# Kernel optimization log

Measured on AMD Instinct MI355X. Metric: run time of the kernel, lower is better.

The kernel has to match this reference:

```python
import jax, jax.numpy as jnp
import numpy as np
import math

EPS = 1e-8
H, DM, S = 16, 1024, 128  # heads, d_model, seq_len (== channels)
DK = DM // H


def _fq_act_uint8(x):
    # Brevitas Uint8ActPerTensorFloat: per-tensor unsigned 8-bit fake-quant (negatives clip to 0)
    s = jnp.maximum(jnp.max(x), EPS) / 255.0
    return jnp.clip(jnp.round(x / s), 0.0, 255.0) * s


def _fq_w_int8(w):
    # Int8 weight per-tensor, narrow range [-127, 127]
    s = jnp.maximum(jnp.max(jnp.abs(w)), EPS) / 127.0
    return jnp.clip(jnp.round(w / s), -127.0, 127.0) * s, s


def _fq_pc_int8(x, axis):
    # QuantIdentity: signed 8-bit fake-quant, per-channel scale along `axis` (abs-max stats)
    red = tuple(i for i in range(x.ndim) if i != axis)
    s = jnp.maximum(jnp.max(jnp.abs(x), axis=red, keepdims=True), EPS) / 127.0
    return jnp.clip(jnp.round(x / s), -128.0, 127.0) * s


def _quant_linear(x, W, b):
    # QuantLinear: uint8 input quant, int8 weight quant, Int32 bias quant (scale = s_in * s_w)
    s_in = jnp.maximum(jnp.max(x), EPS) / 255.0
    xq = jnp.clip(jnp.round(x / s_in), 0.0, 255.0) * s_in
    Wq, s_w = _fq_w_int8(W)
    s_b = s_in * s_w
    bq = jnp.round(b / s_b) * s_b
    return jnp.einsum('bsd,od->bso', xq, Wq) + bq


def setup_inputs() -> dict:
    key = jax.random.key(0)
    ks = jax.random.split(key, 12)
    B = 64
    std = 1.0 / math.sqrt(DM)
    inp = {
        'query': jax.random.normal(ks[0], (B, S, DM), jnp.float32),
        'key':   jax.random.normal(ks[1], (B, S, DM), jnp.float32),
        'value': jax.random.normal(ks[2], (B, S, DM), jnp.float32),
        'mask':  jnp.ones((B, S, S), jnp.int32),
    }
    for i, nm in enumerate(['q', 'k', 'v', 'o']):
        inp[f'W{nm}'] = jax.random.normal(ks[3 + i], (DM, DM), jnp.float32) * std
        inp[f'b{nm}'] = jax.random.normal(ks[7 + i], (DM,), jnp.float32) * 0.01
    return inp


def reference(query, key, value, mask, Wq, bq, Wk, bk, Wv, bv, Wo, bo):
    B = query.shape[0]
    # QuantLinear projections -> [B, h, S, d_k]
    def proj(x, W, b):
        return _quant_linear(x, W, b).reshape(B, S, H, DK).transpose(0, 2, 1, 3)
    q = proj(query, Wq, bq)
    k = proj(key, Wk, bk)
    v = proj(value, Wv, bv)

    # quantizer_1: per-channel on q rows (axis 2); quantizer_2: on k^T columns (axis 3)
    kt = jnp.swapaxes(k, -2, -1)  # [B, h, d_k, S]
    scores = jnp.matmul(_fq_pc_int8(q, 2), _fq_pc_int8(kt, 3)) / math.sqrt(DK)
    scores = jnp.where(mask[:, None, :, :] == 0, -1e9, scores)
    p_attn = jax.nn.softmax(scores, axis=-1)

    # quantizer_3: per-channel on p_attn columns (axis 3); quantizer_4: on v rows (axis 2)
    x = jnp.matmul(_fq_pc_int8(p_attn, 3), _fq_pc_int8(v, 2))  # [B, h, S, d_k]
    x = x.transpose(0, 2, 1, 3).reshape(B, S, DM)
    return _quant_linear(x, Wo, bo)
```

## Files before the change

kernel.cpp:

```cpp
#include <hip/hip_runtime.h>
#include <hip/hip_bf16.h>
#include <math.h>

typedef unsigned short u16;
typedef unsigned int u32;
typedef unsigned long long u64;
typedef signed char i8;

constexpr int NB = 64, NS = 128, NDM = 1024, NH = 16, NDK = 64;
constexpr int NM = NB * NS;
constexpr float QEPS = 1e-8f;

typedef __attribute__((ext_vector_type(8))) short short8;
typedef __attribute__((ext_vector_type(4))) float f32x4;
typedef __attribute__((ext_vector_type(4))) int i32x4;

__device__ __forceinline__ u32 fenc(float f) {
  u32 u = __float_as_uint(f);
  return (u & 0x80000000u) ? ~u : (u | 0x80000000u);
}
__device__ __forceinline__ float fdec(u32 u) {
  u = (u & 0x80000000u) ? (u & 0x7FFFFFFFu) : ~u;
  return __uint_as_float(u);
}
__device__ __forceinline__ u16 f2bf(float f) { return (u16)(__float_as_uint(f) >> 16); }
__device__ __forceinline__ float bf2f(u16 u) { return __uint_as_float(((u32)u) << 16); }

__device__ __forceinline__ void glds16(const void* g, void* l) {
  __builtin_amdgcn_global_load_lds(
      (const __attribute__((address_space(1))) void*)(unsigned long long)(uintptr_t)g,
      (__attribute__((address_space(3))) void*)(u32)(uintptr_t)l, 16, 0, 0);
}


__global__ void maskbits_kernel(const int* __restrict__ mask, u64* __restrict__ mb,
                                u32* __restrict__ scl) {
  if (blockIdx.x == 0) {
    for (int i = threadIdx.x; i < 2048; i += blockDim.x) scl[i] = 0u;
  }
  int row = blockIdx.x * 4 + (threadIdx.x >> 6);
  int lane = threadIdx.x & 63;
  const int* mrow = mask + (size_t)row * NS;
  u64 b0 = __ballot(mrow[lane] != 0);
  u64 b1 = __ballot(mrow[64 + lane] != 0);
  if (lane == 0) { mb[row * 2] = b0; mb[row * 2 + 1] = b1; }
}

__global__ void fused_max_kernel(const float* __restrict__ q, const float* __restrict__ k,
                                 const float* __restrict__ v, const float* __restrict__ w0,
                                 const float* __restrict__ w1, const float* __restrict__ w2,
                                 const float* __restrict__ w3, u32* __restrict__ sclu) {
  int y = blockIdx.y;
  const float* src; size_t n4; int ab;
  switch (y) {
    case 0: src = q; n4 = (size_t)NM * NDM / 4; ab = 0; break;
    case 1: src = k; n4 = (size_t)NM * NDM / 4; ab = 0; break;
    case 2: src = v; n4 = (size_t)NM * NDM / 4; ab = 0; break;
    case 3: src = w0; n4 = (size_t)NDM * NDM / 4; ab = 1; break;
    case 4: src = w1; n4 = (size_t)NDM * NDM / 4; ab = 1; break;
    case 5: src = w2; n4 = (size_t)NDM * NDM / 4; ab = 1; break;
    default: src = w3; n4 = (size_t)NDM * NDM / 4; ab = 1; break;
  }
  float m = -INFINITY;
  size_t stride = (size_t)gridDim.x * blockDim.x;
  for (size_t i = (size_t)blockIdx.x * blockDim.x + threadIdx.x; i < n4; i += stride) {
    float4 f = ((const float4*)src)[i];
    if (ab) { f.x = fabsf(f.x); f.y = fabsf(f.y); f.z = fabsf(f.z); f.w = fabsf(f.w); }
    m = fmaxf(m, fmaxf(fmaxf(f.x, f.y), fmaxf(f.z, f.w)));
  }
  for (int off = 32; off; off >>= 1) m = fmaxf(m, __shfl_down(m, off));
  __shared__ float sm[4];
  if ((threadIdx.x & 63) == 0) sm[threadIdx.x >> 6] = m;
  __syncthreads();
  if (threadIdx.x == 0) {
    float r = fmaxf(fmaxf(sm[0], sm[1]), fmaxf(sm[2], sm[3]));
    atomicMax(&sclu[y], fenc(r));
  }
}

__global__ __launch_bounds__(256)
void quant_w_i8_kernel(const float* __restrict__ w0, const float* __restrict__ w1,
                       const float* __restrict__ w2, const float* __restrict__ w3,
                       i8* __restrict__ dst, int* __restrict__ colsum,
                       const u32* __restrict__ sclu) {
  int y = blockIdx.y, row = blockIdx.x, tid = threadIdx.x;
  const float* src = (y == 0 ? w0 : y == 1 ? w1 : y == 2 ? w2 : w3) + (size_t)row * NDM;
  float s = fmaxf(fdec(sclu[3 + y]), QEPS) / 127.0f;
  float4 f = ((const float4*)src)[tid];
  int a = (int)fminf(fmaxf(rintf(f.x / s), -127.f), 127.f);
  int b = (int)fminf(fmaxf(rintf(f.y / s), -127.f), 127.f);
  int c = (int)fminf(fmaxf(rintf(f.z / s), -127.f), 127.f);
  int d = (int)fminf(fmaxf(rintf(f.w / s), -127.f), 127.f);
  ((int*)(dst + (size_t)y * NDM * NDM + (size_t)row * NDM))[tid] =
      (a & 255) | ((b & 255) << 8) | ((c & 255) << 16) | ((d & 255) << 24);
  int ssum = a + b + c + d;
  for (int off = 32; off; off >>= 1) ssum += __shfl_down(ssum, off);
  __shared__ int sm[4];
  if ((tid & 63) == 0) sm[tid >> 6] = ssum;
  __syncthreads();
  if (tid == 0) colsum[y * NDM + row] = sm[0] + sm[1] + sm[2] + sm[3];
}

__global__ void quant_a_kernel(const float* __restrict__ s0, const float* __restrict__ s1,
                               const float* __restrict__ s2, i8* __restrict__ dst,
                               const u32* __restrict__ sclu, int slot_base) {
  int y = blockIdx.y;
  const float* src = y == 0 ? s0 : y == 1 ? s1 : s2;
  i8* d = dst + (size_t)y * NM * NDM;
  float s = fmaxf(fdec(sclu[slot_base + y]), QEPS) / 255.0f;
  size_t n4 = (size_t)NM * NDM / 4;
  size_t stride = (size_t)gridDim.x * blockDim.x;
  for (size_t i = (size_t)blockIdx.x * blockDim.x + threadIdx.x; i < n4; i += stride) {
    float4 f = ((const float4*)src)[i];
    int a = (int)fminf(fmaxf(rintf(f.x / s), 0.f), 255.f) - 128;
    int b = (int)fminf(fmaxf(rintf(f.y / s), 0.f), 255.f) - 128;
    int c = (int)fminf(fmaxf(rintf(f.z / s), 0.f), 255.f) - 128;
    int e = (int)fminf(fmaxf(rintf(f.w / s), 0.f), 255.f) - 128;
    ((int*)d)[i] = (a & 255) | ((b & 255) << 8) | ((c & 255) << 16) | ((e & 255) << 24);
  }
}

__global__ void qkv_i8_kernel(const float* __restrict__ projbase, i8* __restrict__ dstbase,
                              const float* __restrict__ scl) {
  int y = blockIdx.y;
  const float* src = projbase + (size_t)y * NM * NDM;
  i8* dst = dstbase + (size_t)y * NM * NDM;
  const float* sb = scl + 8 + y * 128;
  size_t n4 = (size_t)NM * NDM / 4;
  size_t stride = (size_t)gridDim.x * blockDim.x;
  for (size_t i = (size_t)blockIdx.x * blockDim.x + threadIdx.x; i < n4; i += stride) {
    int s_idx = (int)((i >> 8) & 127);
    float s = fmaxf(sb[s_idx], QEPS) / 127.0f;
    float4 f = ((const float4*)src)[i];
    int a = (int)fminf(fmaxf(rintf(f.x / s), -128.f), 127.f);
    int b = (int)fminf(fmaxf(rintf(f.y / s), -128.f), 127.f);
    int c = (int)fminf(fmaxf(rintf(f.z / s), -128.f), 127.f);
    int d = (int)fminf(fmaxf(rintf(f.w / s), -128.f), 127.f);
    ((int*)dst)[i] = (a & 255) | ((b & 255) << 8) | ((c & 255) << 16) | ((d & 255) << 24);
  }
}

constexpr int BM = 128, BN = 64, BK = 64, KTILES = NDM / BK;

template <bool PROJ>
__global__ __launch_bounds__(256, 4)
void gemm_kernel(const i8* __restrict__ Abase, const i8* __restrict__ Wbase,
                 const int* __restrict__ colsum, const float* __restrict__ b0,
                 const float* __restrict__ b1, const float* __restrict__ b2,
                 float* __restrict__ Cbase, u32* __restrict__ sclu,
                 float* __restrict__ rmax_part) {
  constexpr int K = NDM, N = NDM;
  const int z = PROJ ? blockIdx.z : 0;
  const i8* A = Abase + (size_t)z * NM * NDM;
  const i8* Wt = PROJ ? (Wbase + (size_t)z * NDM * NDM) : Wbase;
  const float* bias = PROJ ? (z == 0 ? b0 : z == 1 ? b1 : b2) : b0;
  float* C = PROJ ? (Cbase + (size_t)z * NM * NDM) : Cbase;
  const u32* slot_in = PROJ ? (sclu + z) : (sclu + 7);
  const u32* slot_w = PROJ ? (sclu + 3 + z) : (sclu + 6);
  const int* cs = colsum + (PROJ ? z : 3) * NDM;

  __shared__ __align__(16) i8 As[2][BM][BK];
  __shared__ __align__(16) i8 Bs[2][BN][BK];
  __shared__ float rmax2[4][64];

  const int tid = threadIdx.x;
  const int lane = tid & 63, wave = tid >> 6;
  const int wm = (wave & 1) * 64, wn = (wave >> 1) * 32;
  const int r16 = lane & 15, quad = lane >> 4;
  const int bm = blockIdx.x * BM, bn = blockIdx.y * BN;

  const int lrow = lane >> 2, lcol = (lane & 3) * 16;
  const i8* Ab = A + (size_t)(bm + wave * 32 + lrow) * K + lcol;
  const i8* Bb = Wt + (size_t)(bn + wave * 16 + lrow) * K + lcol;

  i32x4 acc[4][2] = {};

  glds16(Ab, &As[0][wave * 32][0]);
  glds16(Ab + (size_t)16 * K, &As[0][wave * 32 + 16][0]);
  glds16(Bb, &Bs[0][wave * 16][0]);
  __syncthreads();

  int cur = 0;
  for (int t = 0; t < KTILES; t++) {
    if (t + 1 < KTILES) {
      int k0 = (t + 1) * BK;
      glds16(Ab + k0, &As[cur ^ 1][wave * 32][0]);
      glds16(Ab + (size_t)16 * K + k0, &As[cur ^ 1][wave * 32 + 16][0]);
      glds16(Bb + k0, &Bs[cur ^ 1][wave * 16][0]);
    }
    i32x4 af[4], bfr[2];
#pragma unroll
    for (int i = 0; i < 4; i++)
      af[i] = *(const i32x4*)(&As[cur][wm + i * 16 + r16][quad * 16]);
#pragma unroll
    for (int j = 0; j < 2; j++)
      bfr[j] = *(const i32x4*)(&Bs[cur][wn + j * 16 + r16][quad * 16]);
#pragma unroll
    for (int i = 0; i < 4; i++)
#pragma unroll
      for (int j = 0; j < 2; j++)
        acc[i][j] = __builtin_amdgcn_mfma_i32_16x16x64_i8(af[i], bfr[j], acc[i][j], 0, 0, 0);
    __syncthreads();
    cur ^= 1;
  }

  float s_in = fmaxf(fdec(*slot_in), QEPS) / 255.0f;
  float s_w = fmaxf(fdec(*slot_w), QEPS) / 127.0f;
  float sc = s_in * s_w;

  float bq[2];
  int csj[2];
#pragma unroll
  for (int j = 0; j < 2; j++) {
    int gc = bn + wn + j * 16 + r16;
    bq[j] = rintf(bias[gc] / sc) * sc;
    csj[j] = cs[gc] << 7;
  }
#pragma unroll
  for (int i = 0; i < 4; i++) {
#pragma unroll
    for (int r = 0; r < 4; r++) {
      int l64 = i * 16 + quad * 4 + r;
      int gr = bm + wm + l64;
      float rm = 0.0f;
#pragma unroll
      for (int j = 0; j < 2; j++) {
        int gc = bn + wn + j * 16 + r16;
        float val = (float)(acc[i][j][r] + csj[j]) * sc + bq[j];
        C[(size_t)gr * N + gc] = val;
        if (PROJ) rm = fmaxf(rm, fabsf(val));
      }
      if (PROJ) {
#pragma unroll
        for (int off = 1; off < 16; off <<= 1) rm = fmaxf(rm, __shfl_xor(rm, off));
        if (r16 == 0) rmax2[wave][l64] = rm;
      }
    }
  }
  if (PROJ) {
    __syncthreads();
    if (tid < BM) {
      int g = tid >> 6, l = tid & 63;
      float m = fmaxf(rmax2[g][l], rmax2[g + 2][l]);
      int blockId = z * 1024 + blockIdx.x * 16 + blockIdx.y;
      rmax_part[(size_t)blockId * 128 + tid] = m;
    }
  }
}

__global__ void rmax_reduce_kernel(const float* __restrict__ part, u32* __restrict__ sclu) {
  int slot = blockIdx.x;
  int z = slot >> 7, lr = slot & 127;
  const float* base = part + (size_t)z * 1024 * 128 + lr;
  float m = 0.0f;
  for (int i = threadIdx.x; i < 1024; i += blockDim.x) m = fmaxf(m, base[(size_t)i * 128]);
  for (int off = 32; off; off >>= 1) m = fmaxf(m, __shfl_down(m, off));
  __shared__ float sm[4];
  if ((threadIdx.x & 63) == 0) sm[threadIdx.x >> 6] = m;
  __syncthreads();
  if (threadIdx.x == 0)
    sclu[8 + slot] = __float_as_uint(fmaxf(fmaxf(sm[0], sm[1]), fmaxf(sm[2], sm[3])));
}

__global__ __launch_bounds__(256)
void attn_colmax_kernel(const i8* __restrict__ qi8, const i8* __restrict__ ki8,
                        const u64* __restrict__ mb, const float* __restrict__ scl,
                        float* __restrict__ cm_part) {
  const int bh = blockIdx.x, b = bh >> 4, h = bh & 15;
  const int tid = threadIdx.x, lane = tid & 63, wave = tid >> 6;
  const int r16 = lane & 15, quad = lane >> 4;

  __shared__ __align__(16) i8 Qs[NS][80];
  __shared__ __align__(16) i8 Ks[NS][80];
  __shared__ float sqv[NS], skv[NS];
  __shared__ float cmw[4][NS];

  {
    int row = tid >> 1, half = (tid & 1) * 32;
    const i8* qp = qi8 + (size_t)(b * NS + row) * NDM + h * NDK + half;
    const i8* kp = ki8 + (size_t)(b * NS + row) * NDM + h * NDK + half;
    *(int4*)&Qs[row][half] = *(const int4*)qp;
    *(int4*)&Qs[row][half + 16] = *(const int4*)(qp + 16);
    *(int4*)&Ks[row][half] = *(const int4*)kp;
    *(int4*)&Ks[row][half + 16] = *(const int4*)(kp + 16);
    if (tid < NS) {
      sqv[tid] = fmaxf(scl[8 + tid], QEPS) / 127.0f;
      skv[tid] = fmaxf(scl[8 + 128 + tid], QEPS) / 127.0f;
    }
  }
  __syncthreads();

  const int rowbase = wave * 32;
  i32x4 acc[2][8] = {};
#pragma unroll
  for (int mt = 0; mt < 2; mt++) {
    i32x4 a = *(const i32x4*)&Qs[rowbase + mt * 16 + r16][quad * 16];
#pragma unroll
    for (int nt = 0; nt < 8; nt++) {
      i32x4 bfrag = *(const i32x4*)&Ks[nt * 16 + r16][quad * 16];
      acc[mt][nt] = __builtin_amdgcn_mfma_i32_16x16x64_i8(a, bfrag, acc[mt][nt], 0, 0, 0);
    }
  }

  float skc[8], cm[8];
#pragma unroll
  for (int nt = 0; nt < 8; nt++) { skc[nt] = skv[nt * 16 + r16]; cm[nt] = 0.0f; }

#pragma unroll
  for (int mt = 0; mt < 2; mt++) {
#pragma unroll
    for (int r = 0; r < 4; r++) {
      int row = rowbase + mt * 16 + quad * 4 + r;
      float sq = sqv[row];
      const u64* mrow = mb + ((size_t)b * NS + row) * 2;
      u64 m0 = mrow[0], m1 = mrow[1];
      float vals[8];
      float mx = -INFINITY;
#pragma unroll
      for (int nt = 0; nt < 8; nt++) {
        float v = (float)acc[mt][nt][r] * (sq * skc[nt]) * 0.125f;
        u64 bits = nt < 4 ? m0 : m1;
        if (((bits >> ((nt * 16 + r16) & 63)) & 1ull) == 0) v = -1e9f;
        vals[nt] = v;
        mx = fmaxf(mx, v);
      }
#pragma unroll
      for (int off = 1; off < 16; off <<= 1) mx = fmaxf(mx, __shfl_xor(mx, off));
      float sum = 0.0f;
#pragma unroll
      for (int nt = 0; nt < 8; nt++) { vals[nt] = __expf(vals[nt] - mx); sum += vals[nt]; }
#pragma unroll
      for (int off = 1; off < 16; off <<= 1) sum += __shfl_xor(sum, off);
#pragma unroll
      for (int nt = 0; nt < 8; nt++) {
        float p = vals[nt] / sum;
        cm[nt] = fmaxf(cm[nt], p);
      }
    }
  }

#pragma unroll
  for (int nt = 0; nt < 8; nt++) {
    float c = cm[nt];
    c = fmaxf(c, __shfl_xor(c, 16));
    c = fmaxf(c, __shfl_xor(c, 32));
    if (quad == 0) cmw[wave][nt * 16 + r16] = c;
  }
  __syncthreads();
  if (tid < NS) {
    float c = fmaxf(fmaxf(cmw[0][tid], cmw[1][tid]), fmaxf(cmw[2][tid], cmw[3][tid]));
    cm_part[(size_t)tid * (NB * NH) + bh] = c;
  }
}

__global__ void colmax_reduce_kernel(const float* __restrict__ cm_part,
                                     u32* __restrict__ sclu) {
  int j = blockIdx.x;
  const float* row = cm_part + (size_t)j * (NB * NH);
  float m = 0.0f;
  for (int i = threadIdx.x; i < NB * NH; i += blockDim.x) m = fmaxf(m, row[i]);
  for (int off = 32; off; off >>= 1) m = fmaxf(m, __shfl_down(m, off));
  __shared__ float sm[4];
  if ((threadIdx.x & 63) == 0) sm[threadIdx.x >> 6] = m;
  __syncthreads();
  if (threadIdx.x == 0)
    sclu[392 + j] = __float_as_uint(fmaxf(fmaxf(sm[0], sm[1]), fmaxf(sm[2], sm[3])));
}

__global__ __launch_bounds__(256, 4)
void attn_pv2_kernel(const i8* __restrict__ qi8, const i8* __restrict__ ki8,
                     const i8* __restrict__ vi8, const u64* __restrict__ mb,
                     const float* __restrict__ scl, float* __restrict__ xout,
                     u32* __restrict__ xmax_slot) {
  const int bh = blockIdx.x, b = bh >> 4, h = bh & 15;
  const int tid = threadIdx.x, lane = tid & 63, wave = tid >> 6;
  const int r16 = lane & 15, quad = lane >> 4;
  const int rowbase = wave * 32;

  union SU {
    i8 K[NS][64];
    struct { u16 hi[64][72]; u16 lo[64][72]; } v;
  };
  __shared__ __align__(16) SU u;
  __shared__ __align__(16) u16 Ps[NS][72];
  __shared__ float sqv[NS], skv[NS], spv[NS], svv[NS];
  __shared__ float xmw[4];

  const int jl = tid >> 2, d0v = (tid & 3) * 16;
  const i8* vb = vi8 + (size_t)(b * NS + jl) * NDM + h * NDK + d0v;
  int4 vpre0 = *(const int4*)vb;
  int4 vpre1 = *(const int4*)(vb + (size_t)64 * NDM);

  i32x4 aq[2];
  {
    const i8* qp = qi8 + (size_t)b * NS * NDM + h * NDK;
#pragma unroll
    for (int mt = 0; mt < 2; mt++)
      aq[mt] = *(const i32x4*)(qp + (size_t)(rowbase + mt * 16 + r16) * NDM + quad * 16);
    const int lrow = lane >> 2, lcol = (lane & 3) * 16;
#pragma unroll
    for (int p = 0; p < 2; p++) {
      int r = wave * 32 + p * 16;
      glds16(ki8 + (size_t)(b * NS + r + lrow) * NDM + h * NDK + lcol, &u.K[r][0]);
    }
    if (tid < NS) {
      sqv[tid] = fmaxf(scl[8 + tid], QEPS) / 127.0f;
      skv[tid] = fmaxf(scl[8 + 128 + tid], QEPS) / 127.0f;
      spv[tid] = fmaxf(scl[392 + tid], QEPS) / 127.0f;
      svv[tid] = fmaxf(scl[8 + 256 + tid], QEPS) / 127.0f;
    }
  }
  __syncthreads();

  i32x4 acc[2][8] = {};
  __builtin_amdgcn_s_setprio(1);
#pragma unroll
  for (int mt = 0; mt < 2; mt++) {
#pragma unroll
    for (int nt = 0; nt < 8; nt++) {
      i32x4 bfrag = *(const i32x4*)&u.K[nt * 16 + r16][quad * 16];
      acc[mt][nt] = __builtin_amdgcn_mfma_i32_16x16x64_i8(aq[mt], bfrag, acc[mt][nt], 0, 0, 0);
    }
  }
  __builtin_amdgcn_s_setprio(0);

  float skc[8], spc[8];
#pragma unroll
  for (int nt = 0; nt < 8; nt++) {
    skc[nt] = skv[nt * 16 + r16];
    spc[nt] = spv[nt * 16 + r16];
  }

  u32 pqh[2][4][2];
#pragma unroll
  for (int mt = 0; mt < 2; mt++) {
#pragma unroll
    for (int r = 0; r < 4; r++) {
      int row = rowbase + mt * 16 + quad * 4 + r;
      float sq = sqv[row];
      const u64* mrow = mb + ((size_t)b * NS + row) * 2;
      u64 m0 = mrow[0], m1 = mrow[1];
      float vals[8];
      float mx = -INFINITY;
#pragma unroll
      for (int nt = 0; nt < 8; nt++) {
        float v = (float)acc[mt][nt][r] * (sq * skc[nt]) * 0.125f;
        u64 bits = nt < 4 ? m0 : m1;
        if (((bits >> ((nt * 16 + r16) & 63)) & 1ull) == 0) v = -1e9f;
        vals[nt] = v;
        mx = fmaxf(mx, v);
      }
#pragma unroll
      for (int off = 1; off < 16; off <<= 1) mx = fmaxf(mx, __shfl_xor(mx, off));
      float sum = 0.0f;
#pragma unroll
      for (int nt = 0; nt < 8; nt++) { vals[nt] = __expf(vals[nt] - mx); sum += vals[nt]; }
#pragma unroll
      for (int off = 1; off < 16; off <<= 1) sum += __shfl_xor(sum, off);
#pragma unroll
      for (int nt = 0; nt < 4; nt++) {
        float p = vals[nt] / sum;
        float pq = fminf(fmaxf(rintf(p / spc[nt]), -128.f), 127.f);
        Ps[row][nt * 16 + r16] = f2bf(pq);
      }
#pragma unroll
      for (int n2 = 0; n2 < 2; n2++) {
        float pa_ = vals[4 + n2 * 2] / sum;
        float pb_ = vals[5 + n2 * 2] / sum;
        float qa = fminf(fmaxf(rintf(pa_ / spc[4 + n2 * 2]), -128.f), 127.f);
        float qb = fminf(fmaxf(rintf(pb_ / spc[5 + n2 * 2]), -128.f), 127.f);
        pqh[mt][r][n2] = (u32)f2bf(qa) | ((u32)f2bf(qb) << 16);
      }
    }
  }

  f32x4 xacc[2][4] = {};
#pragma unroll
  for (int half = 0; half < 2; half++) {
    __syncthreads();
    {
      int j = half * 64 + jl;
      float g = spv[j] * svv[j];
      int4 raw = half ? vpre1 : vpre0;
      const i8* rb = (const i8*)&raw;
#pragma unroll
      for (int d = 0; d < 16; d++) {
        float w = (float)rb[d] * g;
        u16 hi = f2bf(w);
        u.v.hi[d0v + d][jl] = hi;
        u.v.lo[d0v + d][jl] = f2bf(w - bf2f(hi));
      }
    }
    __syncthreads();
    __builtin_amdgcn_s_setprio(1);
#pragma unroll
    for (int kk = 0; kk < 2; kk++) {
      short8 pa[2];
#pragma unroll
      for (int mt = 0; mt < 2; mt++)
        pa[mt] = *(const short8*)&Ps[rowbase + mt * 16 + r16][kk * 32 + quad * 8];
#pragma unroll
      for (int nt = 0; nt < 4; nt++) {
        short8 vh = *(const short8*)&u.v.hi[nt * 16 + r16][kk * 32 + quad * 8];
        short8 vl = *(const short8*)&u.v.lo[nt * 16 + r16][kk * 32 + quad * 8];
#pragma unroll
        for (int mt = 0; mt < 2; mt++) {
          xacc[mt][nt] = __builtin_amdgcn_mfma_f32_16x16x32_bf16(pa[mt], vh, xacc[mt][nt], 0, 0, 0);
          xacc[mt][nt] = __builtin_amdgcn_mfma_f32_16x16x32_bf16(pa[mt], vl, xacc[mt][nt], 0, 0, 0);
        }
      }
    }
    __builtin_amdgcn_s_setprio(0);
    if (half == 0) {
#pragma unroll
      for (int mt = 0; mt < 2; mt++)
#pragma unroll
        for (int r = 0; r < 4; r++) {
          int row = rowbase + mt * 16 + quad * 4 + r;
#pragma unroll
          for (int n2 = 0; n2 < 2; n2++) {
            u32 pk = pqh[mt][r][n2];
            Ps[row][(n2 * 2) * 16 + r16] = (u16)(pk & 0xFFFFu);
            Ps[row][(n2 * 2 + 1) * 16 + r16] = (u16)(pk >> 16);
          }
        }
    }
  }

  float mx = -INFINITY;
#pragma unroll
  for (int mt = 0; mt < 2; mt++)
#pragma unroll
    for (int nt = 0; nt < 4; nt++)
#pragma unroll
      for (int r = 0; r < 4; r++) {
        int row = rowbase + mt * 16 + quad * 4 + r;
        xout[((size_t)b * NS + row) * NDM + h * NDK + nt * 16 + r16] = xacc[mt][nt][r];
        mx = fmaxf(mx, xacc[mt][nt][r]);
      }
#pragma unroll
  for (int off = 1; off < 64; off <<= 1) mx = fmaxf(mx, __shfl_xor(mx, off));
  if (lane == 0) xmw[wave] = mx;
  __syncthreads();
  if (tid == 0) {
    float m = fmaxf(fmaxf(xmw[0], xmw[1]), fmaxf(xmw[2], xmw[3]));
    atomicMax(xmax_slot, fenc(m));
  }
}

constexpr size_t OFF_SCL = 0;
constexpr size_t OFF_CS  = 8192;
constexpr size_t OFF_MB  = OFF_CS + 4 * NDM * 4;
constexpr size_t OFF_W   = OFF_MB + (size_t)NM * 16;
constexpr size_t OFF_XQ  = OFF_W + 4 * (size_t)NDM * NDM;
constexpr size_t OFF_PQ  = OFF_XQ + 3 * (size_t)NM * NDM;
constexpr size_t OFF_I8  = OFF_PQ + 3 * (size_t)NM * NDM * 4;
constexpr size_t OFF_CM  = OFF_I8 + 3 * (size_t)NM * NDM;
constexpr size_t OFF_RP  = OFF_CM + (size_t)NS * NB * NH * 4;

extern "C" void kernel_launch(void* const* d_in, const int* in_sizes, int n_in,
                              void* d_out, int out_size, void* d_ws, size_t ws_size,
                              hipStream_t stream) {
  const float* query = (const float*)d_in[0];
  const float* key = (const float*)d_in[1];
  const float* value = (const float*)d_in[2];
  const int* mask = (const int*)d_in[3];
  const float* Wq = (const float*)d_in[4]; const float* bq = (const float*)d_in[5];
  const float* Wk = (const float*)d_in[6]; const float* bk = (const float*)d_in[7];
  const float* Wv = (const float*)d_in[8]; const float* bv = (const float*)d_in[9];
  const float* Wo = (const float*)d_in[10]; const float* bo = (const float*)d_in[11];

  char* ws = (char*)d_ws;
  float* scl = (float*)(ws + OFF_SCL);
  u32* sclu = (u32*)scl;
  int* colsum = (int*)(ws + OFF_CS);
  u64* mb = (u64*)(ws + OFF_MB);
  i8* wb = (i8*)(ws + OFF_W);
  i8* wob = wb + 3 * (size_t)NDM * NDM;
  i8* xq = (i8*)(ws + OFF_XQ);
  float* proj = (float*)(ws + OFF_PQ);
  i8* qkv8 = (i8*)(ws + OFF_I8);
  float* cm_part = (float*)(ws + OFF_CM);
  float* rmax_part = (float*)(ws + OFF_RP);
  float* xout = proj + 2 * (size_t)NM * NDM;
  i8* vi8 = qkv8 + 2 * (size_t)NM * NDM;

  maskbits_kernel<<<NM / 4, 256, 0, stream>>>(mask, mb, sclu);
  fused_max_kernel<<<dim3(512, 7), 256, 0, stream>>>(query, key, value, Wq, Wk, Wv, Wo, sclu);
  quant_w_i8_kernel<<<dim3(NDM, 4), 256, 0, stream>>>(Wq, Wk, Wv, Wo, wb, colsum, sclu);
  quant_a_kernel<<<dim3(512, 3), 256, 0, stream>>>(query, key, value, xq, sclu, 0);

  gemm_kernel<true><<<dim3(NM / BM, NDM / BN, 3), 256, 0, stream>>>(
      xq, wb, colsum, bq, bk, bv, proj, sclu, rmax_part);
  rmax_reduce_kernel<<<384, 256, 0, stream>>>(rmax_part, sclu);

  qkv_i8_kernel<<<dim3(512, 3), 256, 0, stream>>>(proj, qkv8, scl);

  attn_colmax_kernel<<<NB * NH, 256, 0, stream>>>(qkv8, qkv8 + (size_t)NM * NDM, mb, scl,
                                                  cm_part);
  colmax_reduce_kernel<<<NS, 256, 0, stream>>>(cm_part, sclu);
  attn_pv2_kernel<<<NB * NH, 256, 0, stream>>>(qkv8, qkv8 + (size_t)NM * NDM, vi8, mb, scl,
                                               xout, sclu + 7);

  quant_a_kernel<<<dim3(512, 1), 256, 0, stream>>>(xout, xout, xout, xq, sclu, 7);
  gemm_kernel<false><<<dim3(NM / BM, NDM / BN, 1), 256, 0, stream>>>(
      xq, wob, colsum, bo, bo, bo, (float*)d_out, sclu, rmax_part);
}
```

Measured before the change: 390.9 us.

## Fuse attention colmax, reduce, and PV into one cooperative kernel

Replaces the three attention launches (QK colmax, column-max reduce, PV) with a single cooperative kernel that keeps QK^T probabilities in registers across two grid-wide syncs. This avoids recomputing QK^T and softmax in the PV pass and removes two kernel launches. The cost is grid synchronization overhead and a requirement that all 1024 blocks be co-resident (at least 4 per CU). If that fails, the old three-kernel path is used.

```diff
diff --git a/kernel.cpp b/kernel.cpp
--- a/kernel.cpp
+++ b/kernel.cpp
@@ -1,6 +1,9 @@
 #include <hip/hip_runtime.h>
 #include <hip/hip_bf16.h>
+#include <hip/hip_cooperative_groups.h>
 #include <math.h>
+
+namespace cg = cooperative_groups;
 
 typedef unsigned short u16;
 typedef unsigned int u32;
@@ -262,6 +265,243 @@
     sclu[8 + slot] = __float_as_uint(fmaxf(fmaxf(sm[0], sm[1]), fmaxf(sm[2], sm[3])));
 }
 
+__global__ __launch_bounds__(256, 4)
+void attn_fused_kernel(const i8* __restrict__ qi8, const i8* __restrict__ ki8,
+                       const i8* __restrict__ vi8, const u64* __restrict__ mb,
+                       const float* __restrict__ scl, u32* __restrict__ sclu,
+                       float* __restrict__ cm_part, float* __restrict__ xout,
+                       u32* __restrict__ xmax_slot) {
+  const int bh = blockIdx.x, b = bh >> 4, h = bh & 15;
+  const int tid = threadIdx.x, lane = tid & 63, wave = tid >> 6;
+  const int r16 = lane & 15, quad = lane >> 4;
+  const int rowbase = wave * 32;
+
+  union SU {
+    struct { i8 K[NS][64]; float cmw[4][NS]; } qk;
+    struct { u16 hi[64][72]; u16 lo[64][72]; } v;
+  };
+  __shared__ __align__(16) SU u;
+  __shared__ __align__(16) u16 Ps[NS][72];
+  __shared__ float sqv[NS], skv[NS], svv[NS], spv[NS];
+  __shared__ float xmw[4];
+
+  const int jl = tid >> 2, d0v = (tid & 3) * 16;
+  const i8* vb = vi8 + (size_t)(b * NS + jl) * NDM + h * NDK + d0v;
+  int4 vpre0 = *(const int4*)vb;
+  int4 vpre1 = *(const int4*)(vb + (size_t)64 * NDM);
+
+  i32x4 aq[2];
+  {
+    const i8* qp = qi8 + (size_t)b * NS * NDM + h * NDK;
+#pragma unroll
+    for (int mt = 0; mt < 2; mt++)
+      aq[mt] = *(const i32x4*)(qp + (size_t)(rowbase + mt * 16 + r16) * NDM + quad * 16);
+    const int lrow = lane >> 2, lcol = (lane & 3) * 16;
+#pragma unroll
+    for (int p = 0; p < 2; p++) {
+      int r = wave * 32 + p * 16;
+      glds16(ki8 + (size_t)(b * NS + r + lrow) * NDM + h * NDK + lcol, &u.qk.K[r][0]);
+    }
+    if (tid < NS) {
+      sqv[tid] = fmaxf(scl[8 + tid], QEPS) / 127.0f;
+      skv[tid] = fmaxf(scl[8 + 128 + tid], QEPS) / 127.0f;
+      svv[tid] = fmaxf(scl[8 + 256 + tid], QEPS) / 127.0f;
+    }
+  }
+  __syncthreads();
+
+  i32x4 acc[2][8] = {};
+  __builtin_amdgcn_s_setprio(1);
+#pragma unroll
+  for (int mt = 0; mt < 2; mt++) {
+#pragma unroll
+    for (int nt = 0; nt < 8; nt++) {
+      i32x4 bfrag = *(const i32x4*)&u.qk.K[nt * 16 + r16][quad * 16];
+      acc[mt][nt] = __builtin_amdgcn_mfma_i32_16x16x64_i8(aq[mt], bfrag, acc[mt][nt], 0, 0, 0);
+    }
+  }
+  __builtin_amdgcn_s_setprio(0);
+
+  float skc[8];
+#pragma unroll
+  for (int nt = 0; nt < 8; nt++) skc[nt] = skv[nt * 16 + r16];
+
+  float p[2][4][8];
+  float cm[8] = {0.f, 0.f, 0.f, 0.f, 0.f, 0.f, 0.f, 0.f};
+#pragma unroll
+  for (int mt = 0; mt < 2; mt++) {
+#pragma unroll
+    for (int r = 0; r < 4; r++) {
+      int row = rowbase + mt * 16 + quad * 4 + r;
+      float sq = sqv[row];
+      const u64* mrow = mb + ((size_t)b * NS + row) * 2;
+      u64 m0 = mrow[0], m1 = mrow[1];
+      float vals[8];
+      float mx = -INFINITY;
+#pragma unroll
+      for (int nt = 0; nt < 8; nt++) {
+        float v = (float)acc[mt][nt][r] * (sq * skc[nt]) * 0.125f;
+        u64 bits = nt < 4 ? m0 : m1;
+        if (((bits >> ((nt * 16 + r16) & 63)) & 1ull) == 0) v = -1e9f;
+        vals[nt] = v;
+        mx = fmaxf(mx, v);
+      }
+#pragma unroll
+      for (int off = 1; off < 16; off <<= 1) mx = fmaxf(mx, __shfl_xor(mx, off));
+      float sum = 0.0f;
+#pragma unroll
+      for (int nt = 0; nt < 8; nt++) { vals[nt] = __expf(vals[nt] - mx); sum += vals[nt]; }
+#pragma unroll
+      for (int off = 1; off < 16; off <<= 1) sum += __shfl_xor(sum, off);
+#pragma unroll
+      for (int nt = 0; nt < 8; nt++) {
+        float pv_ = vals[nt] / sum;
+        p[mt][r][nt] = pv_;
+        cm[nt] = fmaxf(cm[nt], pv_);
+      }
+    }
+  }
+
+#pragma unroll
+  for (int nt = 0; nt < 8; nt++) {
+    float c = cm[nt];
+    c = fmaxf(c, __shfl_xor(c, 16));
+    c = fmaxf(c, __shfl_xor(c, 32));
+    if (quad == 0) u.qk.cmw[wave][nt * 16 + r16] = c;
+  }
+  __syncthreads();
+  if (tid < NS) {
+    float c = fmaxf(fmaxf(u.qk.cmw[0][tid], u.qk.cmw[1][tid]),
+                    fmaxf(u.qk.cmw[2][tid], u.qk.cmw[3][tid]));
+    __hip_atomic_store(&cm_part[(size_t)bh * NS + tid], c, __ATOMIC_RELAXED,
+                       __HIP_MEMORY_SCOPE_AGENT);
+  }
+
+  cg::this_grid().sync();
+
+  if (bh < NS) {
+    float m = 0.0f;
+    for (int i = tid; i < NB * NH; i += 256)
+      m = fmaxf(m, __hip_atomic_load(&cm_part[(size_t)i * NS + bh], __ATOMIC_RELAXED,
+                                     __HIP_MEMORY_SCOPE_AGENT));
+#pragma unroll
+    for (int off = 32; off; off >>= 1) m = fmaxf(m, __shfl_down(m, off));
+    if (lane == 0) xmw[wave] = m;
+    __syncthreads();
+    if (tid == 0) {
+      float mm = fmaxf(fmaxf(xmw[0], xmw[1]), fmaxf(xmw[2], xmw[3]));
+      __hip_atomic_store(&sclu[1024 + bh], __float_as_uint(mm), __ATOMIC_RELAXED,
+                         __HIP_MEMORY_SCOPE_AGENT);
+    }
+  }
+
+  cg::this_grid().sync();
+
+  if (tid < NS) {
+    u32 cu = __hip_atomic_load(&sclu[1024 + tid], __ATOMIC_RELAXED,
+                               __HIP_MEMORY_SCOPE_AGENT);
+    spv[tid] = fmaxf(__uint_as_float(cu), QEPS) / 127.0f;
+  }
+  __syncthreads();
+
+  float spc[8];
+#pragma unroll
+  for (int nt = 0; nt < 8; nt++) spc[nt] = spv[nt * 16 + r16];
+
+  u32 pqh[2][4][2];
+#pragma unroll
+  for (int mt = 0; mt < 2; mt++) {
+#pragma unroll
+    for (int r = 0; r < 4; r++) {
+      int row = rowbase + mt * 16 + quad * 4 + r;
+#pragma unroll
+      for (int nt = 0; nt < 4; nt++) {
+        float pq = fminf(fmaxf(rintf(p[mt][r][nt] / spc[nt]), -128.f), 127.f);
+        Ps[row][nt * 16 + r16] = f2bf(pq);
+      }
+#pragma unroll
+      for (int n2 = 0; n2 < 2; n2++) {
+        float qa = fminf(fmaxf(rintf(p[mt][r][4 + n2 * 2] / spc[4 + n2 * 2]), -128.f), 127.f);
+        float qb = fminf(fmaxf(rintf(p[mt][r][5 + n2 * 2] / spc[5 + n2 * 2]), -128.f), 127.f);
+        pqh[mt][r][n2] = (u32)f2bf(qa) | ((u32)f2bf(qb) << 16);
+      }
+    }
+  }
+
+  f32x4 xacc[2][4] = {};
+#pragma unroll
+  for (int half = 0; half < 2; half++) {
+    __syncthreads();
+    {
+      int j = half * 64 + jl;
+      float g = spv[j] * svv[j];
+      int4 raw = half ? vpre1 : vpre0;
+      const i8* rb = (const i8*)&raw;
+#pragma unroll
+      for (int d = 0; d < 16; d++) {
+        float w = (float)rb[d] * g;
+        u16 hi = f2bf(w);
+        u.v.hi[d0v + d][jl] = hi;
+        u.v.lo[d0v + d][jl] = f2bf(w - bf2f(hi));
+      }
+    }
+    __syncthreads();
+    __builtin_amdgcn_s_setprio(1);
+#pragma unroll
+    for (int kk = 0; kk < 2; kk++) {
+      short8 pa[2];
+#pragma unroll
+      for (int mt = 0; mt < 2; mt++)
+        pa[mt] = *(const short8*)&Ps[rowbase + mt * 16 + r16][kk * 32 + quad * 8];
+#pragma unroll
+      for (int nt = 0; nt < 4; nt++) {
+        short8 vh = *(const short8*)&u.v.hi[nt * 16 + r16][kk * 32 + quad * 8];
+        short8 vl = *(const short8*)&u.v.lo[nt * 16 + r16][kk * 32 + quad * 8];
+#pragma unroll
+        for (int mt = 0; mt < 2; mt++) {
+          xacc[mt][nt] = __builtin_amdgcn_mfma_f32_16x16x32_bf16(pa[mt], vh, xacc[mt][nt], 0, 0, 0);
+          xacc[mt][nt] = __builtin_amdgcn_mfma_f32_16x16x32_bf16(pa[mt], vl, xacc[mt][nt], 0, 0, 0);
+        }
+      }
+    }
+    __builtin_amdgcn_s_setprio(0);
+    if (half == 0) {
+#pragma unroll
+      for (int mt = 0; mt < 2; mt++)
+#pragma unroll
+        for (int r = 0; r < 4; r++) {
+          int row = rowbase + mt * 16 + quad * 4 + r;
+#pragma unroll
+          for (int n2 = 0; n2 < 2; n2++) {
+            u32 pk = pqh[mt][r][n2];
+            Ps[row][(n2 * 2) * 16 + r16] = (u16)(pk & 0xFFFFu);
+            Ps[row][(n2 * 2 + 1) * 16 + r16] = (u16)(pk >> 16);
+          }
+        }
+    }
+  }
+
+  float mx = -INFINITY;
+#pragma unroll
+  for (int mt = 0; mt < 2; mt++)
+#pragma unroll
+    for (int nt = 0; nt < 4; nt++)
+#pragma unroll
+      for (int r = 0; r < 4; r++) {
+        int row = rowbase + mt * 16 + quad * 4 + r;
+        xout[((size_t)b * NS + row) * NDM + h * NDK + nt * 16 + r16] = xacc[mt][nt][r];
+        mx = fmaxf(mx, xacc[mt][nt][r]);
+      }
+#pragma unroll
+  for (int off = 1; off < 64; off <<= 1) mx = fmaxf(mx, __shfl_xor(mx, off));
+  if (lane == 0) xmw[wave] = mx;
+  __syncthreads();
+  if (tid == 0) {
+    float m = fmaxf(fmaxf(xmw[0], xmw[1]), fmaxf(xmw[2], xmw[3]));
+    atomicMax(xmax_slot, fenc(m));
+  }
+}
+
 __global__ __launch_bounds__(256)
 void attn_colmax_kernel(const i8* __restrict__ qi8, const i8* __restrict__ ki8,
                         const u64* __restrict__ mb, const float* __restrict__ scl,
@@ -596,11 +836,36 @@
 
   qkv_i8_kernel<<<dim3(512, 3), 256, 0, stream>>>(proj, qkv8, scl);
 
-  attn_colmax_kernel<<<NB * NH, 256, 0, stream>>>(qkv8, qkv8 + (size_t)NM * NDM, mb, scl,
-                                                  cm_part);
-  colmax_reduce_kernel<<<NS, 256, 0, stream>>>(cm_part, sclu);
-  attn_pv2_kernel<<<NB * NH, 256, 0, stream>>>(qkv8, qkv8 + (size_t)NM * NDM, vi8, mb, scl,
-                                               xout, sclu + 7);
+  static int coop_ok = -1;
+  if (coop_ok < 0) {
+    int nb = 0;
+    hipError_t e = hipOccupancyMaxActiveBlocksPerMultiprocessor(&nb, attn_fused_kernel, 256, 0);
+    coop_ok = (e == hipSuccess && nb >= 4) ? 1 : 0;
+  }
+  bool launched = false;
+  if (coop_ok) {
+    const i8* a_q = qkv8;
+    const i8* a_k = qkv8 + (size_t)NM * NDM;
+    const i8* a_v = vi8;
+    const u64* a_mb = mb;
+    const float* a_scl = scl;
+    u32* a_sclu = sclu;
+    float* a_cm = cm_part;
+    float* a_xout = xout;
+    u32* a_xm = sclu + 7;
+    void* args[] = {&a_q, &a_k, &a_v, &a_mb, &a_scl, &a_sclu, &a_cm, &a_xout, &a_xm};
+    hipError_t e = hipLaunchCooperativeKernel((const void*)attn_fused_kernel,
+                                              dim3(NB * NH), dim3(256), args, 0, stream);
+    launched = (e == hipSuccess);
+    if (!launched) coop_ok = 0;
+  }
+  if (!launched) {
+    attn_colmax_kernel<<<NB * NH, 256, 0, stream>>>(qkv8, qkv8 + (size_t)NM * NDM, mb, scl,
+                                                    cm_part);
+    colmax_reduce_kernel<<<NS, 256, 0, stream>>>(cm_part, sclu);
+    attn_pv2_kernel<<<NB * NH, 256, 0, stream>>>(qkv8, qkv8 + (size_t)NM * NDM, vi8, mb,
+                                                 scl, xout, sclu + 7);
+  }
 
   quant_a_kernel<<<dim3(512, 1), 256, 0, stream>>>(xout, xout, xout, xq, sclu, 7);
   gemm_kernel<false><<<dim3(NM / BM, NDM / BN, 1), 256, 0, stream>>>(
```

After: 384.8 us. About the same (-1.6%).
